# Kernel tuning notes

Measured on AMD Instinct MI355X. Metric: run time of the kernel, lower is better.

## Reference

```python
import jax, jax.numpy as jnp
import numpy as np

B, N, HID = 2, 512, 768
BIAF = 256
CLS = 14
CH = 32
SIZE_DIM = 25
N_POS = 30
HSZ = 2 * (BIAF + 1) + SIZE_DIM


def setup_inputs() -> dict:
    key = jax.random.key(0)
    ks = jax.random.split(key, 16)
    s = 0.02
    return {
        "x": jax.random.normal(ks[0], (B, N, HID), jnp.float32),
        "y": jax.random.normal(ks[1], (B, N, HID), jnp.float32),
        "z": jax.random.normal(ks[2], (B, N, N, CH), jnp.float32),
        "mlp1_w": jax.random.normal(ks[3], (BIAF, HID), jnp.float32) * s,
        "mlp1_b": jnp.zeros((BIAF,), jnp.float32),
        "mlp2_w": jax.random.normal(ks[4], (BIAF, HID), jnp.float32) * s,
        "mlp2_b": jnp.zeros((BIAF,), jnp.float32),
        "head_w": jax.random.normal(ks[5], (BIAF, HID), jnp.float32) * s,
        "head_b": jnp.zeros((BIAF,), jnp.float32),
        "tail_w": jax.random.normal(ks[6], (BIAF, HID), jnp.float32) * s,
        "tail_b": jnp.zeros((BIAF,), jnp.float32),
        "biaf_W": jax.random.normal(ks[7], (CLS, BIAF + 1, BIAF + 1), jnp.float32) * s,
        "W": jax.random.normal(ks[8], (CLS, HSZ), jnp.float32) * s,
        "size_emb": jax.random.normal(ks[9], (N_POS, SIZE_DIM), jnp.float32) * s,
    }


def reference(x, y, z, mlp1_w, mlp1_b, mlp2_w, mlp2_b, head_w, head_b,
              tail_w, tail_b, biaf_W, W, size_emb):
    # MLP branches (dropout=0 at eval; torch GELU is exact erf)
    h = jax.nn.gelu(x @ mlp1_w.T + mlp1_b, approximate=False)   # (b,m,BIAF)
    t = jax.nn.gelu(y @ mlp2_w.T + mlp2_b, approximate=False)   # (b,n,BIAF)
    ones = jnp.ones(h.shape[:-1] + (1,), h.dtype)
    h1 = jnp.concatenate([h, ones], -1)                          # (b,m,BIAF+1)
    t1 = jnp.concatenate([t, ones], -1)                          # (b,n,BIAF+1)
    # Biaffine with bias_x=bias_y=True -> (b,cls,m,n)
    o1 = jnp.einsum('bmi,kij,bnj->bkmn', h1, biaf_W, t1)

    # head/tail MLPs with LeakyReLU(0.01), then append 1-column
    head = jax.nn.leaky_relu(x @ head_w.T + head_b, 0.01)
    tail = jax.nn.leaky_relu(x @ tail_w.T + tail_b, 0.01)
    head = jnp.concatenate([head, ones], -1)                     # (b,m,BIAF+1)
    tail = jnp.concatenate([tail, ones], -1)                     # (b,n,BIAF+1)

    # einsum('bmnh,kh->bkmn', cat([head_m, tail_n, size_mn]), W) decomposed so
    # the (b,m,n,HSZ) pairwise tensor is never materialized (same math).
    d = head.shape[-1]
    Wh, Wt, Ws = W[:, :d], W[:, d:2 * d], W[:, 2 * d:]
    n = x.shape[1]
    ar = jnp.arange(n)
    ids = jnp.clip(ar[None, :] - ar[:, None], -N_POS // 2, N_POS // 2 - 1) + N_POS // 2
    se = size_emb[ids]                                           # (m,n,SIZE_DIM)
    o3 = (jnp.einsum('bmh,kh->bkm', head, Wh)[:, :, :, None]
          + jnp.einsum('bnh,kh->bkn', tail, Wt)[:, :, None, :]
          + jnp.einsum('mnh,kh->kmn', se, Ws)[None])
    return o1 + o3
```

## Files before the change

### kernel.cpp

```cpp
#include <hip/hip_runtime.h>
#include <hip/hip_bf16.h>
#include <math.h>
#include <stdint.h>

#define BDIM 2
#define NDIM 512
#define HID 768
#define BIAF 256
#define CLS 14
#define DD 257
#define NPOS 30
#define SDIM 25
#define HSZ 539
#define PK 288
#define PJ 384

typedef unsigned short ushort_t;
typedef __attribute__((ext_vector_type(8))) short short8;
typedef __attribute__((ext_vector_type(4))) float floatx4;
typedef __attribute__((ext_vector_type(4))) unsigned short ushort4_t;

#define MFMA16(a, b, c) __builtin_amdgcn_mfma_f32_16x16x32_bf16((a), (b), (c), 0, 0, 0)

__device__ inline float bf2f(ushort_t u) {
    union { unsigned int i; float f; } c; c.i = ((unsigned)u) << 16; return c.f;
}
__device__ inline ushort_t f2bf(float f) {
    __hip_bfloat16 h = __float2bfloat16(f);
    return *(ushort_t*)&h;
}

__device__ inline void glds16(const ushort_t* g, const ushort_t* l) {
    __builtin_amdgcn_global_load_lds(
        (const __attribute__((address_space(1))) unsigned int*)(unsigned long long)(uintptr_t)g,
        (__attribute__((address_space(3))) unsigned int*)(unsigned int)(uintptr_t)l,
        16, 0, 0);
}


__global__ __launch_bounds__(256) void repack_t(
    const float* __restrict__ biafW, ushort_t* __restrict__ packW)
{
    __shared__ float tile[32][33];
    const int i0 = blockIdx.x * 32;
    const int j0 = blockIdx.y * 32;
    const int k  = blockIdx.z;
    const int r8 = threadIdx.x >> 5;
    const int c  = threadIdx.x & 31;
    #pragma unroll
    for (int rr = 0; rr < 4; ++rr) {
        int r = rr * 8 + r8;
        int gi = i0 + r, gj = j0 + c;
        tile[r][c] = (gi < DD && gj < DD) ? biafW[((size_t)k * DD + gi) * DD + gj] : 0.f;
    }
    __syncthreads();
    #pragma unroll
    for (int rr = 0; rr < 4; ++rr) {
        int jr = rr * 8 + r8;
        packW[((size_t)k * PJ + (j0 + jr)) * PK + i0 + c] = f2bf(tile[c][jr]);
    }
}

__global__ __launch_bounds__(256) void prep_split(
    const float* __restrict__ x, const float* __restrict__ y,
    const float* __restrict__ m1w, const float* __restrict__ m2w,
    const float* __restrict__ hw,  const float* __restrict__ tw,
    ushort_t* __restrict__ xhi, ushort_t* __restrict__ xlo,
    ushort_t* __restrict__ yhi, ushort_t* __restrict__ ylo,
    ushort_t* __restrict__ whi, ushort_t* __restrict__ wlo,
    ushort_t* __restrict__ h1hi, ushort_t* __restrict__ h1lo,
    ushort_t* __restrict__ t1hi, ushort_t* __restrict__ t1lo)
{
    int tg = blockIdx.x * 256 + threadIdx.x;
    if (tg < 196608) {
        int mat = tg / 49152;
        int e0  = (tg % 49152) * 4;
        const float* src = (mat == 0) ? m1w : (mat == 1) ? m2w : (mat == 2) ? hw : tw;
        float4 v = *(const float4*)(src + e0);
        size_t o = (size_t)mat * 196608 + e0;
        ushort4_t h, lo;
        h[0] = f2bf(v.x); lo[0] = f2bf(v.x - bf2f(h[0]));
        h[1] = f2bf(v.y); lo[1] = f2bf(v.y - bf2f(h[1]));
        h[2] = f2bf(v.z); lo[2] = f2bf(v.z - bf2f(h[2]));
        h[3] = f2bf(v.w); lo[3] = f2bf(v.w - bf2f(h[3]));
        *(ushort4_t*)(whi + o) = h;
        *(ushort4_t*)(wlo + o) = lo;
    } else if (tg < 589824) {
        int t = tg - 196608;
        int which = t / 196608;
        int e0 = (t % 196608) * 4;
        const float* src = which ? y : x;
        float4 v = *(const float4*)(src + e0);
        ushort4_t h, lo;
        h[0] = f2bf(v.x); lo[0] = f2bf(v.x - bf2f(h[0]));
        h[1] = f2bf(v.y); lo[1] = f2bf(v.y - bf2f(h[1]));
        h[2] = f2bf(v.z); lo[2] = f2bf(v.z - bf2f(h[2]));
        h[3] = f2bf(v.w); lo[3] = f2bf(v.w - bf2f(h[3]));
        *(ushort4_t*)((which ? yhi : xhi) + e0) = h;
        *(ushort4_t*)((which ? ylo : xlo) + e0) = lo;
    } else {
        int idx = tg - 589824;
        int plane = idx >> 15;
        int tok = (idx >> 5) & 1023;
        int c   = 256 + (idx & 31);
        ushort_t* dst = (plane == 0) ? h1hi : (plane == 1) ? h1lo : (plane == 2) ? t1hi : t1lo;
        ushort_t val = (c == 256 && (plane == 0 || plane == 2)) ? (ushort_t)0x3F80 : (ushort_t)0;
        dst[(size_t)tok * PK + c] = val;
    }
}

__global__ __launch_bounds__(256) void proj_mfma(
    const ushort_t* __restrict__ xhi, const ushort_t* __restrict__ xlo,
    const ushort_t* __restrict__ yhi, const ushort_t* __restrict__ ylo,
    const ushort_t* __restrict__ whi, const ushort_t* __restrict__ wlo,
    const float* __restrict__ m1b, const float* __restrict__ m2b,
    const float* __restrict__ hb,  const float* __restrict__ tb,
    ushort_t* __restrict__ h1hi, ushort_t* __restrict__ h1lo,
    ushort_t* __restrict__ t1hi, ushort_t* __restrict__ t1lo,
    float* __restrict__ headf, float* __restrict__ tailf)
{
    const int ft = blockIdx.x;
    const int mt = blockIdx.y;
    const int proj = blockIdx.z;
    const int wave = threadIdx.x >> 6, L = threadIdx.x & 63;
    const int quad = L >> 4, l16 = L & 15;
    const int tok0 = mt * 64 + wave * 16;
    const int f0 = ft * 32;

    const ushort_t* ahi_p = (proj == 1) ? yhi : xhi;
    const ushort_t* alo_p = (proj == 1) ? ylo : xlo;
    const float* bias = (proj == 0) ? m1b : (proj == 1) ? m2b : (proj == 2) ? hb : tb;

    const size_t aoff = (size_t)(tok0 + l16) * HID + quad * 8;
    const size_t wbase = (size_t)proj * BIAF * HID;
    const size_t b0 = wbase + (size_t)(f0 + l16) * HID + quad * 8;
    const size_t b1 = wbase + (size_t)(f0 + 16 + l16) * HID + quad * 8;

    floatx4 acc0 = {0.f, 0.f, 0.f, 0.f}, acc1 = {0.f, 0.f, 0.f, 0.f};
    #pragma unroll 4
    for (int k0 = 0; k0 < HID; k0 += 32) {
        short8 ah  = *(const short8*)(ahi_p + aoff + k0);
        short8 al  = *(const short8*)(alo_p + aoff + k0);
        short8 bh0 = *(const short8*)(whi + b0 + k0);
        short8 bl0 = *(const short8*)(wlo + b0 + k0);
        short8 bh1 = *(const short8*)(whi + b1 + k0);
        short8 bl1 = *(const short8*)(wlo + b1 + k0);
        acc0 = MFMA16(ah, bh0, acc0);
        acc1 = MFMA16(ah, bh1, acc1);
        acc0 = MFMA16(al, bh0, acc0);
        acc1 = MFMA16(al, bh1, acc1);
        acc0 = MFMA16(ah, bl0, acc0);
        acc1 = MFMA16(ah, bl1, acc1);
    }

    #pragma unroll
    for (int nf = 0; nf < 2; ++nf) {
        floatx4 a = nf ? acc1 : acc0;
        int feat = f0 + nf * 16 + l16;
        float bv = bias[feat];
        #pragma unroll
        for (int r = 0; r < 4; ++r) {
            int tok = tok0 + quad * 4 + r;
            float v = a[r] + bv;
            if (proj <= 1) {
                float g = 0.5f * v * (1.0f + erff(v * 0.70710678118654752f));
                ushort_t h = f2bf(g);
                ushort_t lo = f2bf(g - bf2f(h));
                if (proj == 0) { h1hi[(size_t)tok * PK + feat] = h; h1lo[(size_t)tok * PK + feat] = lo; }
                else           { t1hi[(size_t)tok * PK + feat] = h; t1lo[(size_t)tok * PK + feat] = lo; }
            } else {
                float lv = (v >= 0.f) ? v : 0.01f * v;
                if (proj == 2) headf[(size_t)tok * 256 + feat] = lv;
                else           tailf[(size_t)tok * 256 + feat] = lv;
            }
        }
    }
}

__global__ __launch_bounds__(256) void hk_tk_sk(
    const float* __restrict__ headf, const float* __restrict__ tailf,
    const float* __restrict__ W, const float* __restrict__ semb,
    float* __restrict__ hk, float* __restrict__ tk, float* __restrict__ skp)
{
    if (blockIdx.x >= 128) {
        int idx = (blockIdx.x - 128) * 256 + threadIdx.x;
        if (idx < CLS * NPOS) {
            int k = idx / NPOS, d = idx % NPOS;
            float acc = 0.f;
            for (int h = 0; h < SDIM; ++h)
                acc += semb[d*SDIM + h] * W[k*HSZ + 2*DD + h];
            skp[idx] = acc;
        }
        return;
    }
    int p = blockIdx.x * 256 + threadIdx.x;
    int which = p >> 14;
    int idx = p & 16383;
    int tok = idx >> 4;
    int k = idx & 15;
    if (k >= CLS) return;
    const float* row = (which ? tailf : headf) + (size_t)tok * 256;
    const float* wr = W + (size_t)k * HSZ + (which ? DD : 0);
    float acc = 0.f;
    for (int f4 = 0; f4 < 64; ++f4) {
        float4 rv = *(const float4*)(row + f4 * 4);
        acc += rv.x * wr[f4*4] + rv.y * wr[f4*4+1] + rv.z * wr[f4*4+2] + rv.w * wr[f4*4+3];
    }
    acc += wr[256];
    float* dst = which ? tk : hk;
    dst[(size_t)(tok >> 9) * CLS * NDIM + (size_t)k * NDIM + (tok & 511)] = acc;
}

__global__ __launch_bounds__(256) void mb_tile(
    const ushort_t* __restrict__ h1hi, const ushort_t* __restrict__ h1lo,
    const ushort_t* __restrict__ packW,
    ushort_t* __restrict__ Ab)
{
    __shared__ ushort_t Ah[64 * 32];
    __shared__ ushort_t Al[64 * 32];
    __shared__ ushort_t Bt[96 * 32];
    const int jt = blockIdx.x, mt = blockIdx.y, bk = blockIdx.z;
    const int b = bk / CLS, k = bk % CLS;
    const int tid = threadIdx.x;
    const int wave = tid >> 6, L = tid & 63;
    const int quad = L >> 4, l16 = L & 15;
    const int sr = L >> 3, u = (L & 7) ^ sr;
    const int srow = 2 * sr + (u >> 2);
    const int scol = (u & 3) * 8;
    const int rbase = (l16 >> 1) * 64 + ((((((l16 & 1) << 2) | quad)) ^ (l16 >> 1)) * 8);
    const int m0 = mt * 64, j0 = jt * 96;
    const int wm = (wave >> 1) * 32, wj = (wave & 1) * 48;

    const ushort_t* gAh = h1hi + (size_t)(b * NDIM + m0) * PK;
    const ushort_t* gAl = h1lo + (size_t)(b * NDIM + m0) * PK;
    const ushort_t* gB  = packW + ((size_t)k * PJ + j0) * PK;

    floatx4 acc[2][3];
    #pragma unroll
    for (int mi = 0; mi < 2; ++mi)
        #pragma unroll
        for (int ni = 0; ni < 3; ++ni)
            #pragma unroll
            for (int r = 0; r < 4; ++r) acc[mi][ni][r] = 0.f;

    for (int k0 = 0; k0 < PK; k0 += 32) {
        for (int s = wave; s < 14; s += 4) {
            const ushort_t* g; const ushort_t* l;
            if (s < 4)      { l = Ah + s * 512;       g = gAh + (size_t)(s * 16 + srow) * PK + k0 + scol; }
            else if (s < 8) { l = Al + (s - 4) * 512; g = gAl + (size_t)((s - 4) * 16 + srow) * PK + k0 + scol; }
            else            { l = Bt + (s - 8) * 512; g = gB  + (size_t)((s - 8) * 16 + srow) * PK + k0 + scol; }
            glds16(g, l);
        }
        __syncthreads();
        short8 ah[2], al[2], bb[3];
        #pragma unroll
        for (int mi = 0; mi < 2; ++mi) {
            ah[mi] = *(const short8*)(Ah + (wm + mi * 16) * 32 + rbase);
            al[mi] = *(const short8*)(Al + (wm + mi * 16) * 32 + rbase);
        }
        #pragma unroll
        for (int ni = 0; ni < 3; ++ni)
            bb[ni] = *(const short8*)(Bt + (wj + ni * 16) * 32 + rbase);
        #pragma unroll
        for (int mi = 0; mi < 2; ++mi)
            #pragma unroll
            for (int ni = 0; ni < 3; ++ni) {
                acc[mi][ni] = MFMA16(ah[mi], bb[ni], acc[mi][ni]);
                acc[mi][ni] = MFMA16(al[mi], bb[ni], acc[mi][ni]);
            }
        __syncthreads();
    }

    ushort_t* Aout = Ab + (size_t)bk * NDIM * PK;
    #pragma unroll
    for (int mi = 0; mi < 2; ++mi) {
        #pragma unroll
        for (int r = 0; r < 4; ++r) {
            int row = m0 + wm + mi * 16 + quad * 4 + r;
            #pragma unroll
            for (int ni = 0; ni < 3; ++ni) {
                int col = j0 + wj + ni * 16 + l16;
                Aout[(size_t)row * PK + col] = f2bf(acc[mi][ni][r]);
            }
        }
    }
}

__global__ __launch_bounds__(256) void mo_tile(
    const ushort_t* __restrict__ Ab,
    const ushort_t* __restrict__ t1hi, const ushort_t* __restrict__ t1lo,
    const float* __restrict__ hk, const float* __restrict__ tk,
    const float* __restrict__ sk,
    float* __restrict__ out)
{
    __shared__ ushort_t At[64 * 32];
    __shared__ ushort_t Bh[128 * 32];
    __shared__ ushort_t Bl[128 * 32];
    __shared__ float skr[NPOS];
    const int nt = blockIdx.x, mt = blockIdx.y, bk = blockIdx.z;
    const int b = bk / CLS, k = bk % CLS;
    const int tid = threadIdx.x;
    if (tid < NPOS) skr[tid] = sk[k * NPOS + tid];
    const int wave = tid >> 6, L = tid & 63;
    const int quad = L >> 4, l16 = L & 15;
    const int sr = L >> 3, u = (L & 7) ^ sr;
    const int srow = 2 * sr + (u >> 2);
    const int scol = (u & 3) * 8;
    const int rbase = (l16 >> 1) * 64 + ((((((l16 & 1) << 2) | quad)) ^ (l16 >> 1)) * 8);
    const int m0 = mt * 64, n0 = nt * 128;
    const int wm = (wave >> 1) * 32, wn = (wave & 1) * 64;

    const ushort_t* gA  = Ab + ((size_t)bk * NDIM + m0) * PK;
    const ushort_t* gBh = t1hi + (size_t)(b * NDIM + n0) * PK;
    const ushort_t* gBl = t1lo + (size_t)(b * NDIM + n0) * PK;

    floatx4 acc[2][4];
    #pragma unroll
    for (int mi = 0; mi < 2; ++mi)
        #pragma unroll
        for (int ni = 0; ni < 4; ++ni)
            #pragma unroll
            for (int r = 0; r < 4; ++r) acc[mi][ni][r] = 0.f;

    for (int k0 = 0; k0 < PK; k0 += 32) {
        for (int s = wave; s < 20; s += 4) {
            const ushort_t* g; const ushort_t* l;
            if (s < 4)       { l = At + s * 512;        g = gA  + (size_t)(s * 16 + srow) * PK + k0 + scol; }
            else if (s < 12) { l = Bh + (s - 4) * 512;  g = gBh + (size_t)((s - 4) * 16 + srow) * PK + k0 + scol; }
            else             { l = Bl + (s - 12) * 512; g = gBl + (size_t)((s - 12) * 16 + srow) * PK + k0 + scol; }
            glds16(g, l);
        }
        __syncthreads();
        short8 a[2], bh[4], bl[4];
        #pragma unroll
        for (int mi = 0; mi < 2; ++mi)
            a[mi] = *(const short8*)(At + (wm + mi * 16) * 32 + rbase);
        #pragma unroll
        for (int ni = 0; ni < 4; ++ni) {
            bh[ni] = *(const short8*)(Bh + (wn + ni * 16) * 32 + rbase);
            bl[ni] = *(const short8*)(Bl + (wn + ni * 16) * 32 + rbase);
        }
        #pragma unroll
        for (int mi = 0; mi < 2; ++mi)
            #pragma unroll
            for (int ni = 0; ni < 4; ++ni) {
                acc[mi][ni] = MFMA16(a[mi], bh[ni], acc[mi][ni]);
                acc[mi][ni] = MFMA16(a[mi], bl[ni], acc[mi][ni]);
            }
        __syncthreads();
    }

    const size_t obase = (size_t)bk * NDIM;
    #pragma unroll
    for (int mi = 0; mi < 2; ++mi) {
        #pragma unroll
        for (int r = 0; r < 4; ++r) {
            int row = m0 + wm + mi * 16 + quad * 4 + r;
            float hv = hk[obase + row];
            #pragma unroll
            for (int ni = 0; ni < 4; ++ni) {
                int col = n0 + wn + ni * 16 + l16;
                int d = col - row; d = d < -15 ? -15 : (d > 14 ? 14 : d); d += 15;
                out[(obase + row) * NDIM + col] = acc[mi][ni][r] + hv + tk[obase + col] + skr[d];
            }
        }
    }
}

extern "C" void kernel_launch(void* const* d_in, const int* in_sizes, int n_in,
                              void* d_out, int out_size, void* d_ws, size_t ws_size,
                              hipStream_t stream) {
    const float* x    = (const float*)d_in[0];
    const float* y    = (const float*)d_in[1];
    const float* m1w  = (const float*)d_in[3];
    const float* m1b  = (const float*)d_in[4];
    const float* m2w  = (const float*)d_in[5];
    const float* m2b  = (const float*)d_in[6];
    const float* hw   = (const float*)d_in[7];
    const float* hb   = (const float*)d_in[8];
    const float* tw   = (const float*)d_in[9];
    const float* tb   = (const float*)d_in[10];
    const float* biafW= (const float*)d_in[11];
    const float* W    = (const float*)d_in[12];
    const float* semb = (const float*)d_in[13];

    char* p = (char*)d_ws;
    float* hk   = (float*)p;                    p += 57344;
    float* tk   = (float*)p;                    p += 57344;
    float* skp  = (float*)p;                    p += 2048;
    float* headf= (float*)p;                    p += 1048576;
    float* tailf= (float*)p;                    p += 1048576;
    ushort_t* h1hi = (ushort_t*)p;              p += 589824;
    ushort_t* h1lo = (ushort_t*)p;              p += 589824;
    ushort_t* t1hi = (ushort_t*)p;              p += 589824;
    ushort_t* t1lo = (ushort_t*)p;              p += 589824;
    ushort_t* packW= (ushort_t*)p;              p += 3096576;
    ushort_t* whi  = (ushort_t*)p;              p += 1572864;
    ushort_t* wlo  = (ushort_t*)p;              p += 1572864;
    ushort_t* Abuf = (ushort_t*)p;              p += 8257536;
    ushort_t* xhi  = (ushort_t*)p;              p += 1572864;
    ushort_t* xlo  = (ushort_t*)p;              p += 1572864;
    ushort_t* yhi  = (ushort_t*)p;              p += 1572864;
    ushort_t* ylo  = (ushort_t*)p;              p += 1572864;

    repack_t<<<dim3(9, 12, CLS), 256, 0, stream>>>(biafW, packW);
    prep_split<<<2816, 256, 0, stream>>>(x, y, m1w, m2w, hw, tw,
                                         xhi, xlo, yhi, ylo, whi, wlo,
                                         h1hi, h1lo, t1hi, t1lo);
    proj_mfma<<<dim3(8, 16, 4), 256, 0, stream>>>(xhi, xlo, yhi, ylo, whi, wlo,
                                                  m1b, m2b, hb, tb,
                                                  h1hi, h1lo, t1hi, t1lo, headf, tailf);
    hk_tk_sk<<<130, 256, 0, stream>>>(headf, tailf, W, semb, hk, tk, skp);
    mb_tile<<<dim3(3, 8, BDIM*CLS), 256, 0, stream>>>(h1hi, h1lo, packW, Abuf);
    mo_tile<<<dim3(4, 8, BDIM*CLS), 256, 0, stream>>>(Abuf, t1hi, t1lo, hk, tk, skp,
                                                      (float*)d_out);
}
```

Before: 204.8 us.

## Merge independent launches and double-buffer LDS tiles in biaffine GEMMs

Folds the biaffine weight repack into the input-split kernel, and the hk/tk/sk projection into the mb_tile GEMM, by giving each branch its own range of block indices. This removes two kernel launches and lets independent work share a grid. Both MFMA GEMM kernels now double-buffer their LDS tiles, issuing the global-to-LDS loads for the next K slice before computing the current one. The cost is twice the LDS per block, which may lower occupancy.

```diff
diff --git a/kernel.cpp b/kernel.cpp
--- a/kernel.cpp
+++ b/kernel.cpp
@@ -38,30 +38,8 @@
 }
 
 
-__global__ __launch_bounds__(256) void repack_t(
-    const float* __restrict__ biafW, ushort_t* __restrict__ packW)
-{
-    __shared__ float tile[32][33];
-    const int i0 = blockIdx.x * 32;
-    const int j0 = blockIdx.y * 32;
-    const int k  = blockIdx.z;
-    const int r8 = threadIdx.x >> 5;
-    const int c  = threadIdx.x & 31;
-    #pragma unroll
-    for (int rr = 0; rr < 4; ++rr) {
-        int r = rr * 8 + r8;
-        int gi = i0 + r, gj = j0 + c;
-        tile[r][c] = (gi < DD && gj < DD) ? biafW[((size_t)k * DD + gi) * DD + gj] : 0.f;
-    }
-    __syncthreads();
-    #pragma unroll
-    for (int rr = 0; rr < 4; ++rr) {
-        int jr = rr * 8 + r8;
-        packW[((size_t)k * PJ + (j0 + jr)) * PK + i0 + c] = f2bf(tile[c][jr]);
-    }
-}
-
-__global__ __launch_bounds__(256) void prep_split(
+__global__ __launch_bounds__(256) void prep_all(
+    const float* __restrict__ biafW, ushort_t* __restrict__ packW,
     const float* __restrict__ x, const float* __restrict__ y,
     const float* __restrict__ m1w, const float* __restrict__ m2w,
     const float* __restrict__ hw,  const float* __restrict__ tw,
@@ -71,7 +49,30 @@
     ushort_t* __restrict__ h1hi, ushort_t* __restrict__ h1lo,
     ushort_t* __restrict__ t1hi, ushort_t* __restrict__ t1lo)
 {
-    int tg = blockIdx.x * 256 + threadIdx.x;
+    const int bid = blockIdx.x;
+    if (bid < 1512) {
+        __shared__ float tile[32][33];
+        const int ix = bid % 9;
+        const int jy = (bid / 9) % 12;
+        const int k  = bid / 108;
+        const int i0 = ix * 32, j0 = jy * 32;
+        const int r8 = threadIdx.x >> 5;
+        const int c  = threadIdx.x & 31;
+        #pragma unroll
+        for (int rr = 0; rr < 4; ++rr) {
+            int r = rr * 8 + r8;
+            int gi = i0 + r, gj = j0 + c;
+            tile[r][c] = (gi < DD && gj < DD) ? biafW[((size_t)k * DD + gi) * DD + gj] : 0.f;
+        }
+        __syncthreads();
+        #pragma unroll
+        for (int rr = 0; rr < 4; ++rr) {
+            int jr = rr * 8 + r8;
+            packW[((size_t)k * PJ + (j0 + jr)) * PK + i0 + c] = f2bf(tile[c][jr]);
+        }
+        return;
+    }
+    int tg = (bid - 1512) * 256 + threadIdx.x;
     if (tg < 196608) {
         int mat = tg / 49152;
         int e0  = (tg % 49152) * 4;
@@ -177,49 +178,51 @@
     }
 }
 
-__global__ __launch_bounds__(256) void hk_tk_sk(
+__global__ __launch_bounds__(256) void mb_hk(
+    const ushort_t* __restrict__ h1hi, const ushort_t* __restrict__ h1lo,
+    const ushort_t* __restrict__ packW,
+    ushort_t* __restrict__ Ab,
     const float* __restrict__ headf, const float* __restrict__ tailf,
     const float* __restrict__ W, const float* __restrict__ semb,
     float* __restrict__ hk, float* __restrict__ tk, float* __restrict__ skp)
 {
-    if (blockIdx.x >= 128) {
-        int idx = (blockIdx.x - 128) * 256 + threadIdx.x;
-        if (idx < CLS * NPOS) {
-            int k = idx / NPOS, d = idx % NPOS;
-            float acc = 0.f;
-            for (int h = 0; h < SDIM; ++h)
-                acc += semb[d*SDIM + h] * W[k*HSZ + 2*DD + h];
-            skp[idx] = acc;
-        }
+    const int bid = blockIdx.x;
+    if (bid >= 672) {
+        const int hb = bid - 672;
+        if (hb >= 128) {
+            int idx = (hb - 128) * 256 + threadIdx.x;
+            if (idx < CLS * NPOS) {
+                int k = idx / NPOS, d = idx % NPOS;
+                float acc = 0.f;
+                for (int h = 0; h < SDIM; ++h)
+                    acc += semb[d*SDIM + h] * W[k*HSZ + 2*DD + h];
+                skp[idx] = acc;
+            }
+            return;
+        }
+        int p = hb * 256 + threadIdx.x;
+        int which = p >> 14;
+        int idx = p & 16383;
+        int tok = idx >> 4;
+        int k = idx & 15;
+        if (k >= CLS) return;
+        const float* row = (which ? tailf : headf) + (size_t)tok * 256;
+        const float* wr = W + (size_t)k * HSZ + (which ? DD : 0);
+        float acc = 0.f;
+        for (int f4 = 0; f4 < 64; ++f4) {
+            float4 rv = *(const float4*)(row + f4 * 4);
+            acc += rv.x * wr[f4*4] + rv.y * wr[f4*4+1] + rv.z * wr[f4*4+2] + rv.w * wr[f4*4+3];
+        }
+        acc += wr[256];
+        float* dst = which ? tk : hk;
+        dst[(size_t)(tok >> 9) * CLS * NDIM + (size_t)k * NDIM + (tok & 511)] = acc;
         return;
     }
-    int p = blockIdx.x * 256 + threadIdx.x;
-    int which = p >> 14;
-    int idx = p & 16383;
-    int tok = idx >> 4;
-    int k = idx & 15;
-    if (k >= CLS) return;
-    const float* row = (which ? tailf : headf) + (size_t)tok * 256;
-    const float* wr = W + (size_t)k * HSZ + (which ? DD : 0);
-    float acc = 0.f;
-    for (int f4 = 0; f4 < 64; ++f4) {
-        float4 rv = *(const float4*)(row + f4 * 4);
-        acc += rv.x * wr[f4*4] + rv.y * wr[f4*4+1] + rv.z * wr[f4*4+2] + rv.w * wr[f4*4+3];
-    }
-    acc += wr[256];
-    float* dst = which ? tk : hk;
-    dst[(size_t)(tok >> 9) * CLS * NDIM + (size_t)k * NDIM + (tok & 511)] = acc;
-}
-
-__global__ __launch_bounds__(256) void mb_tile(
-    const ushort_t* __restrict__ h1hi, const ushort_t* __restrict__ h1lo,
-    const ushort_t* __restrict__ packW,
-    ushort_t* __restrict__ Ab)
-{
-    __shared__ ushort_t Ah[64 * 32];
-    __shared__ ushort_t Al[64 * 32];
-    __shared__ ushort_t Bt[96 * 32];
-    const int jt = blockIdx.x, mt = blockIdx.y, bk = blockIdx.z;
+
+    __shared__ ushort_t Ah[2 * 2048];
+    __shared__ ushort_t Al[2 * 2048];
+    __shared__ ushort_t Bt[2 * 3072];
+    const int jt = bid % 3, mt = (bid / 3) % 8, bk = bid / 24;
     const int b = bk / CLS, k = bk % CLS;
     const int tid = threadIdx.x;
     const int wave = tid >> 6, L = tid & 63;
@@ -235,6 +238,16 @@
     const ushort_t* gAl = h1lo + (size_t)(b * NDIM + m0) * PK;
     const ushort_t* gB  = packW + ((size_t)k * PJ + j0) * PK;
 
+    auto stage = [&](int bo, int k0) {
+        for (int s = wave; s < 14; s += 4) {
+            const ushort_t* g; const ushort_t* l;
+            if (s < 4)      { l = Ah + bo * 2048 + s * 512;       g = gAh + (size_t)(s * 16 + srow) * PK + k0 + scol; }
+            else if (s < 8) { l = Al + bo * 2048 + (s - 4) * 512; g = gAl + (size_t)((s - 4) * 16 + srow) * PK + k0 + scol; }
+            else            { l = Bt + bo * 3072 + (s - 8) * 512; g = gB  + (size_t)((s - 8) * 16 + srow) * PK + k0 + scol; }
+            glds16(g, l);
+        }
+    };
+
     floatx4 acc[2][3];
     #pragma unroll
     for (int mi = 0; mi < 2; ++mi)
@@ -243,24 +256,20 @@
             #pragma unroll
             for (int r = 0; r < 4; ++r) acc[mi][ni][r] = 0.f;
 
-    for (int k0 = 0; k0 < PK; k0 += 32) {
-        for (int s = wave; s < 14; s += 4) {
-            const ushort_t* g; const ushort_t* l;
-            if (s < 4)      { l = Ah + s * 512;       g = gAh + (size_t)(s * 16 + srow) * PK + k0 + scol; }
-            else if (s < 8) { l = Al + (s - 4) * 512; g = gAl + (size_t)((s - 4) * 16 + srow) * PK + k0 + scol; }
-            else            { l = Bt + (s - 8) * 512; g = gB  + (size_t)((s - 8) * 16 + srow) * PK + k0 + scol; }
-            glds16(g, l);
-        }
-        __syncthreads();
+    stage(0, 0);
+    __syncthreads();
+    int cur = 0;
+    for (int t = 0; t < 9; ++t) {
+        if (t < 8) stage(cur ^ 1, (t + 1) * 32);
         short8 ah[2], al[2], bb[3];
         #pragma unroll
         for (int mi = 0; mi < 2; ++mi) {
-            ah[mi] = *(const short8*)(Ah + (wm + mi * 16) * 32 + rbase);
-            al[mi] = *(const short8*)(Al + (wm + mi * 16) * 32 + rbase);
+            ah[mi] = *(const short8*)(Ah + cur * 2048 + (wm + mi * 16) * 32 + rbase);
+            al[mi] = *(const short8*)(Al + cur * 2048 + (wm + mi * 16) * 32 + rbase);
         }
         #pragma unroll
         for (int ni = 0; ni < 3; ++ni)
-            bb[ni] = *(const short8*)(Bt + (wj + ni * 16) * 32 + rbase);
+            bb[ni] = *(const short8*)(Bt + cur * 3072 + (wj + ni * 16) * 32 + rbase);
         #pragma unroll
         for (int mi = 0; mi < 2; ++mi)
             #pragma unroll
@@ -269,6 +278,7 @@
                 acc[mi][ni] = MFMA16(al[mi], bb[ni], acc[mi][ni]);
             }
         __syncthreads();
+        cur ^= 1;
     }
 
     ushort_t* Aout = Ab + (size_t)bk * NDIM * PK;
@@ -293,9 +303,9 @@
     const float* __restrict__ sk,
     float* __restrict__ out)
 {
-    __shared__ ushort_t At[64 * 32];
-    __shared__ ushort_t Bh[128 * 32];
-    __shared__ ushort_t Bl[128 * 32];
+    __shared__ ushort_t At[2 * 2048];
+    __shared__ ushort_t Bh[2 * 4096];
+    __shared__ ushort_t Bl[2 * 4096];
     __shared__ float skr[NPOS];
     const int nt = blockIdx.x, mt = blockIdx.y, bk = blockIdx.z;
     const int b = bk / CLS, k = bk % CLS;
@@ -314,6 +324,16 @@
     const ushort_t* gBh = t1hi + (size_t)(b * NDIM + n0) * PK;
     const ushort_t* gBl = t1lo + (size_t)(b * NDIM + n0) * PK;
 
+    auto stage = [&](int bo, int k0) {
+        for (int s = wave; s < 20; s += 4) {
+            const ushort_t* g; const ushort_t* l;
+            if (s < 4)       { l = At + bo * 2048 + s * 512;         g = gA  + (size_t)(s * 16 + srow) * PK + k0 + scol; }
+            else if (s < 12) { l = Bh + bo * 4096 + (s - 4) * 512;   g = gBh + (size_t)((s - 4) * 16 + srow) * PK + k0 + scol; }
+            else             { l = Bl + bo * 4096 + (s - 12) * 512;  g = gBl + (size_t)((s - 12) * 16 + srow) * PK + k0 + scol; }
+            glds16(g, l);
+        }
+    };
+
     floatx4 acc[2][4];
     #pragma unroll
     for (int mi = 0; mi < 2; ++mi)
@@ -322,23 +342,19 @@
             #pragma unroll
             for (int r = 0; r < 4; ++r) acc[mi][ni][r] = 0.f;
 
-    for (int k0 = 0; k0 < PK; k0 += 32) {
-        for (int s = wave; s < 20; s += 4) {
-            const ushort_t* g; const ushort_t* l;
-            if (s < 4)       { l = At + s * 512;        g = gA  + (size_t)(s * 16 + srow) * PK + k0 + scol; }
-            else if (s < 12) { l = Bh + (s - 4) * 512;  g = gBh + (size_t)((s - 4) * 16 + srow) * PK + k0 + scol; }
-            else             { l = Bl + (s - 12) * 512; g = gBl + (size_t)((s - 12) * 16 + srow) * PK + k0 + scol; }
-            glds16(g, l);
-        }
-        __syncthreads();
+    stage(0, 0);
+    __syncthreads();
+    int cur = 0;
+    for (int t = 0; t < 9; ++t) {
+        if (t < 8) stage(cur ^ 1, (t + 1) * 32);
         short8 a[2], bh[4], bl[4];
         #pragma unroll
         for (int mi = 0; mi < 2; ++mi)
-            a[mi] = *(const short8*)(At + (wm + mi * 16) * 32 + rbase);
+            a[mi] = *(const short8*)(At + cur * 2048 + (wm + mi * 16) * 32 + rbase);
         #pragma unroll
         for (int ni = 0; ni < 4; ++ni) {
-            bh[ni] = *(const short8*)(Bh + (wn + ni * 16) * 32 + rbase);
-            bl[ni] = *(const short8*)(Bl + (wn + ni * 16) * 32 + rbase);
+            bh[ni] = *(const short8*)(Bh + cur * 4096 + (wn + ni * 16) * 32 + rbase);
+            bl[ni] = *(const short8*)(Bl + cur * 4096 + (wn + ni * 16) * 32 + rbase);
         }
         #pragma unroll
         for (int mi = 0; mi < 2; ++mi)
@@ -348,6 +364,7 @@
                 acc[mi][ni] = MFMA16(a[mi], bl[ni], acc[mi][ni]);
             }
         __syncthreads();
+        cur ^= 1;
     }
 
     const size_t obase = (size_t)bk * NDIM;
@@ -403,15 +420,14 @@
     ushort_t* yhi  = (ushort_t*)p;              p += 1572864;
     ushort_t* ylo  = (ushort_t*)p;              p += 1572864;
 
-    repack_t<<<dim3(9, 12, CLS), 256, 0, stream>>>(biafW, packW);
-    prep_split<<<2816, 256, 0, stream>>>(x, y, m1w, m2w, hw, tw,
-                                         xhi, xlo, yhi, ylo, whi, wlo,
-                                         h1hi, h1lo, t1hi, t1lo);
+    prep_all<<<4328, 256, 0, stream>>>(biafW, packW, x, y, m1w, m2w, hw, tw,
+                                       xhi, xlo, yhi, ylo, whi, wlo,
+                                       h1hi, h1lo, t1hi, t1lo);
     proj_mfma<<<dim3(8, 16, 4), 256, 0, stream>>>(xhi, xlo, yhi, ylo, whi, wlo,
                                                   m1b, m2b, hb, tb,
                                                   h1hi, h1lo, t1hi, t1lo, headf, tailf);
-    hk_tk_sk<<<130, 256, 0, stream>>>(headf, tailf, W, semb, hk, tk, skp);
-    mb_tile<<<dim3(3, 8, BDIM*CLS), 256, 0, stream>>>(h1hi, h1lo, packW, Abuf);
+    mb_hk<<<802, 256, 0, stream>>>(h1hi, h1lo, packW, Abuf,
+                                   headf, tailf, W, semb, hk, tk, skp);
     mo_tile<<<dim3(4, 8, BDIM*CLS), 256, 0, stream>>>(Abuf, t1hi, t1lo, hk, tk, skp,
                                                       (float*)d_out);
 }
```

Measured after the change: 199.5 us. -2.6%, faster.
